# Optimization experiments

Hardware: AMD Instinct MI355X
Metric: run time of the kernel (lower is better)

The kernel has to match this reference:

```python
import jax, jax.numpy as jnp
import numpy as np

N = 80000          # nodes
E = 1280000        # edges (~avg degree 16)
D_IN = 64          # Lorentz ambient dim (1 time + 63 spatial feature dims)
D_HID = 64
EPS = 1e-8


def _lorentz_inner(x):
    # <x,x>_L = -x0^2 + ||x_space||^2  (keepdims)
    return -x[:, :1] * x[:, :1] + jnp.sum(x[:, 1:] * x[:, 1:], axis=-1, keepdims=True)


def _to_manifold(s):
    # scale so that <s,s>_L = -1 (curvature c=1 hyperboloid)
    denom = jnp.sqrt(jnp.clip(jnp.abs(_lorentz_inner(s)), EPS))
    return s / denom


def _lorentz_linear(x, W, b, log_scale, nonlin=None):
    # HyboNet LorentzLinear: dense map, then rebuild a valid hyperboloid point
    if nonlin is not None:
        x = nonlin(x)
    h = x @ W.T + b
    time = jax.nn.sigmoid(h[:, :1]) * jnp.exp(log_scale) + 1.1
    space = h[:, 1:]
    sq = jnp.clip(jnp.sum(space * space, axis=-1, keepdims=True), EPS)
    scale = (time * time - 1.0) / sq
    return jnp.concatenate([time, space * jnp.sqrt(scale)], axis=-1)


def _agg(h, src, dst, w):
    # sparse adjacency aggregation (spmm) + Lorentz centroid normalization
    s = jax.ops.segment_sum(w[:, None] * h[src], dst, num_segments=N)
    return _to_manifold(s)


def setup_inputs() -> dict:
    key = jax.random.key(0)
    ks = jax.random.split(key, 6)
    x = jax.random.normal(ks[0], (N, D_IN - 1), jnp.float32)
    edge_index = jax.random.randint(ks[1], (2, E), 0, N, dtype=jnp.int32)
    edge_weight = jax.random.uniform(ks[2], (E,), jnp.float32)
    W1 = jax.random.normal(ks[3], (D_HID, D_IN), jnp.float32) * 0.02
    b1 = jnp.zeros((D_HID,), jnp.float32)
    s1 = jnp.asarray(np.log(10.0), jnp.float32)   # LorentzLinear scale param (log-space)
    W2 = jax.random.normal(ks[4], (D_HID, D_HID), jnp.float32) * 0.02
    b2 = jnp.zeros((D_HID,), jnp.float32)
    s2 = jnp.asarray(np.log(10.0), jnp.float32)
    return dict(x=x, edge_index=edge_index, edge_weight=edge_weight,
                W1=W1, b1=b1, s1=s1, W2=W2, b2=b2, s2=s2)


def reference(x, edge_index, edge_weight, W1, b1, s1, W2, b2, s2):
    src, dst = edge_index[0], edge_index[1]
    n = x.shape[0]
    # lift to Lorentz tangent space at origin: prepend zero time coord
    # (proj_tan0 is then a no-op since time component is already 0)
    u_space = x                                             # [N, D_IN-1]
    # expmap0 (c=1): [cosh(||u||), sinh(||u||) * u/||u||]
    nrm = jnp.clip(jnp.linalg.norm(u_space, axis=-1, keepdims=True), EPS)
    p_space = jnp.sinh(nrm) * u_space / nrm
    # projx: recompute time coord from spatial part, x0 = sqrt(1 + ||x_s||^2)
    p_time = jnp.sqrt(1.0 + jnp.sum(p_space * p_space, axis=-1, keepdims=True))
    p = jnp.concatenate([p_time, p_space], axis=1)          # [N, D_IN]
    # conv1 (no nonlin) and conv2 (relu) = LorentzLinear + Lorentz aggregation
    h1 = _agg(_lorentz_linear(p, W1, b1, s1), src, dst, edge_weight)
    h2 = _agg(_lorentz_linear(h1, W2, b2, s2, nonlin=jax.nn.relu), src, dst, edge_weight)
    # LResNet hyperbolic residual: Lorentz-normalized sum of the two points
    return _to_manifold(h1 + h2)
```

## Files before the change

### kernel.cpp

```cpp
#include <hip/hip_runtime.h>
#include <hip/hip_bf16.h>

#define D 64
#define EPS 1e-8f
#define BSH 10
#define BNODES (1 << BSH)
#define ABLK 4096

typedef __attribute__((ext_vector_type(8))) short bf16x8;
typedef __attribute__((ext_vector_type(4))) float f32x4;

__device__ __forceinline__ float wave_sum64(float v) {
    #pragma unroll
    for (int d = 1; d < 64; d <<= 1) v += __shfl_xor(v, d);
    return v;
}

__device__ __forceinline__ unsigned short f2bf_rn(float f) {
    unsigned u = __float_as_uint(f);
    return (unsigned short)((u + 0x7FFFu + ((u >> 16) & 1u)) >> 16);
}

__device__ __forceinline__ void split8(float4 a, float4 b, bf16x8& h, bf16x8& l) {
    float f[8] = {a.x, a.y, a.z, a.w, b.x, b.y, b.z, b.w};
    #pragma unroll
    for (int i = 0; i < 8; ++i) {
        unsigned u = __float_as_uint(f[i]);
        float hf = __uint_as_float(u & 0xFFFF0000u);
        unsigned lu = __float_as_uint(f[i] - hf);
        h[i] = (short)(u >> 16);
        l[i] = (short)(lu >> 16);
    }
}

__global__ __launch_bounds__(256) void k_bcount(const int* __restrict__ dst,
                                                int* __restrict__ bcnt,
                                                int e, int nbuck) {
    __shared__ int cnt[128];
    int tid = threadIdx.x;
    if (tid < 128) cnt[tid] = 0;
    __syncthreads();
    int i0 = blockIdx.x * 1024 + tid;
    #pragma unroll
    for (int u = 0; u < 4; ++u) {
        int i = i0 + u * 256;
        if (i < e) atomicAdd(&cnt[dst[i] >> BSH], 1);
    }
    __syncthreads();
    if (tid < nbuck && cnt[tid]) atomicAdd(&bcnt[tid], cnt[tid]);
}

__global__ __launch_bounds__(128) void k_bscan(const int* __restrict__ bcnt,
                                               int* __restrict__ bstart,
                                               int* __restrict__ gcur,
                                               int* __restrict__ off,
                                               int n, int e, int nbuck) {
    __shared__ int sm[128];
    int tid = threadIdx.x;
    int v = (tid < nbuck) ? bcnt[tid] : 0;
    sm[tid] = v;
    __syncthreads();
    #pragma unroll
    for (int d = 1; d < 128; d <<= 1) {
        int t = (tid >= d) ? sm[tid - d] : 0;
        __syncthreads();
        sm[tid] += t;
        __syncthreads();
    }
    int excl = sm[tid] - v;
    if (tid < nbuck) { bstart[tid] = excl; gcur[tid] = excl; }
    if (tid == 0) { bstart[nbuck] = e; off[n] = e; }
}

__global__ __launch_bounds__(256) void k_bucketA(const int* __restrict__ src,
                                                 const int* __restrict__ dst,
                                                 const float* __restrict__ w,
                                                 int* __restrict__ gcur,
                                                 unsigned long long* __restrict__ tmp,
                                                 int e, int nbuck) {
    __shared__ int cnt[128];
    __shared__ int base[128];
    int tid = threadIdx.x;
    if (tid < 128) cnt[tid] = 0;
    __syncthreads();
    int i0 = blockIdx.x * ABLK + tid;
    int bkt[16], rnk[16];
    #pragma unroll
    for (int u = 0; u < 16; ++u) {
        int i = i0 + u * 256;
        if (i < e) {
            int b = dst[i] >> BSH;
            bkt[u] = b;
            rnk[u] = atomicAdd(&cnt[b], 1);
        }
    }
    __syncthreads();
    if (tid < 128) {
        int c = cnt[tid];
        base[tid] = c ? atomicAdd(&gcur[tid], c) : 0;
    }
    __syncthreads();
    #pragma unroll
    for (int u = 0; u < 16; ++u) {
        int i = i0 + u * 256;
        if (i < e) {
            unsigned long long pk =
                ((unsigned long long)__float_as_uint(w[i]) << 32)
                | (unsigned int)(src[i] | ((dst[i] & (BNODES - 1)) << 20));
            tmp[base[bkt[u]] + rnk[u]] = pk;
        }
    }
}

__global__ __launch_bounds__(1024) void k_bucketB(const unsigned long long* __restrict__ tmp,
                                                  const int* __restrict__ bstart,
                                                  int* __restrict__ off,
                                                  unsigned long long* __restrict__ epack,
                                                  int n) {
    __shared__ int cur[BNODES];
    __shared__ int sm[BNODES];
    int b = blockIdx.x;
    int v0 = b << BSH;
    int nv = min(BNODES, n - v0);
    int tid = threadIdx.x;
    cur[tid] = 0;
    __syncthreads();
    int s0 = bstart[b], s1 = bstart[b + 1];
    for (int i = s0 + tid; i < s1; i += 1024)
        atomicAdd(&cur[((unsigned)tmp[i] >> 20) & (BNODES - 1)], 1);
    __syncthreads();
    int v = cur[tid];
    sm[tid] = v;
    __syncthreads();
    #pragma unroll
    for (int d = 1; d < BNODES; d <<= 1) {
        int t = (tid >= d) ? sm[tid - d] : 0;
        __syncthreads();
        sm[tid] += t;
        __syncthreads();
    }
    int node_off = s0 + sm[tid] - v;
    if (tid < nv) off[v0 + tid] = node_off;
    cur[tid] = node_off;
    __syncthreads();
    for (int i = s0 + tid; i < s1; i += 1024) {
        unsigned long long pk = tmp[i];
        int dl = ((unsigned)pk >> 20) & (BNODES - 1);
        int pos = atomicAdd(&cur[dl], 1);
        epack[pos] = pk & 0xFFFFFFFFC00FFFFFULL;
    }
}

__global__ __launch_bounds__(256) void k_embed(const float* __restrict__ x,
                                               float* __restrict__ P, int n) {
    int lane = threadIdx.x & 63, wv = threadIdx.x >> 6;
    int node0 = blockIdx.x * 64 + wv * 16;
    int node1 = min(node0 + 16, n);
    for (int node = node0; node < node1; ++node) {
        float xv = (lane >= 1) ? x[(size_t)node * 63 + (lane - 1)] : 0.f;
        float nrm2 = wave_sum64(xv * xv);
        float nrm = fmaxf(sqrtf(nrm2), EPS);
        float sh = sinhf(nrm);
        float ps = sh * xv / nrm;
        float pt = sqrtf(1.f + sh * sh);
        P[(size_t)node * 64 + lane] = (lane == 0) ? pt : ps;
    }
}

template <int RELU>
__global__ __launch_bounds__(256) void k_lin_mfma(const float* __restrict__ tbl,
                                                  const float* __restrict__ W,
                                                  const float* __restrict__ bias,
                                                  const float* __restrict__ sc,
                                                  unsigned short* __restrict__ out, int n) {
    int lane = threadIdx.x & 63, wv = threadIdx.x >> 6;
    int col = lane & 15, grp = lane >> 4;
    int node0 = blockIdx.x * 64 + wv * 16;
    if (node0 >= n) return;

    float es = expf(sc[0]);

    bf16x8 wh[2][4], wl[2][4];
    #pragma unroll
    for (int s = 0; s < 2; ++s)
        #pragma unroll
        for (int t = 0; t < 4; ++t) {
            const float* wp = W + (t * 16 + col) * 64 + s * 32 + grp * 8;
            split8(*(const float4*)wp, *(const float4*)(wp + 4), wh[s][t], wl[s][t]);
        }

    f32x4 acc[4];
    #pragma unroll
    for (int t = 0; t < 4; ++t) {
        float bv = bias[t * 16 + col];
        acc[t] = (f32x4){bv, bv, bv, bv};
    }

    int arow = node0 + col;
    if (arow >= n) arow = n - 1;
    #pragma unroll
    for (int s = 0; s < 2; ++s) {
        const float* ap = tbl + (size_t)arow * 64 + s * 32 + grp * 8;
        float4 a0 = *(const float4*)ap;
        float4 a1 = *(const float4*)(ap + 4);
        if (RELU) {
            a0.x = fmaxf(a0.x, 0.f); a0.y = fmaxf(a0.y, 0.f);
            a0.z = fmaxf(a0.z, 0.f); a0.w = fmaxf(a0.w, 0.f);
            a1.x = fmaxf(a1.x, 0.f); a1.y = fmaxf(a1.y, 0.f);
            a1.z = fmaxf(a1.z, 0.f); a1.w = fmaxf(a1.w, 0.f);
        }
        bf16x8 ah, al;
        split8(a0, a1, ah, al);
        #pragma unroll
        for (int t = 0; t < 4; ++t) {
            acc[t] = __builtin_amdgcn_mfma_f32_16x16x32_bf16(ah, wh[s][t], acc[t], 0, 0, 0);
            acc[t] = __builtin_amdgcn_mfma_f32_16x16x32_bf16(al, wh[s][t], acc[t], 0, 0, 0);
            acc[t] = __builtin_amdgcn_mfma_f32_16x16x32_bf16(ah, wl[s][t], acc[t], 0, 0, 0);
        }
    }

    float tot[4];
    #pragma unroll
    for (int r = 0; r < 4; ++r) {
        float s = 0.f;
        #pragma unroll
        for (int t = 0; t < 4; ++t) s += acc[t][r] * acc[t][r];
        tot[r] = s;
    }
    #pragma unroll
    for (int d2 = 1; d2 < 16; d2 <<= 1) {
        #pragma unroll
        for (int r = 0; r < 4; ++r) tot[r] += __shfl_xor(tot[r], d2);
    }
    float tm[4], rs[4];
    #pragma unroll
    for (int r = 0; r < 4; ++r) {
        float h0 = __shfl(acc[0][r], lane & 48);
        tm[r] = es / (1.f + expf(-h0)) + 1.1f;
        float sq = fmaxf(tot[r] - h0 * h0, EPS);
        rs[r] = sqrtf((tm[r] * tm[r] - 1.f) / sq);
    }
    #pragma unroll
    for (int t = 0; t < 4; ++t) {
        #pragma unroll
        for (int r = 0; r < 4; ++r) {
            int row = node0 + grp * 4 + r;
            if (row < n) {
                int j = t * 16 + col;
                float v = (j == 0) ? tm[r] : acc[t][r] * rs[r];
                out[(size_t)row * 64 + j] = f2bf_rn(v);
            }
        }
    }
}

template <int FINAL>
__global__ __launch_bounds__(256) void k_agg(const unsigned short* __restrict__ t,
                                             const int* __restrict__ off,
                                             const float2* __restrict__ epack,
                                             const float* __restrict__ h1,
                                             float* __restrict__ out, int n) {
    __shared__ __align__(16) float2 ebuf[4][64];
    int lane = threadIdx.x & 63, wv = threadIdx.x >> 6;
    int q = lane >> 4, sub = lane & 15;
    int node = blockIdx.x * 4 + wv;
    if (node >= n) return;
    int s0 = off[node], s1 = off[node + 1];
    float ax = 0.f, ay = 0.f, az = 0.f, aw = 0.f;
    for (int base = s0; base < s1; base += 64) {
        int c = min(s1 - base, 64);
        float2 ev = (lane < c) ? epack[base + lane] : make_float2(0.f, 0.f);
        ebuf[wv][lane] = ev;
        int c4 = (c + 3) & ~3;
        for (int j = 0; j < c4; j += 4) {
            float2 e = ebuf[wv][j + q];
            int src = __float_as_int(e.x);
            float w = e.y;
            const unsigned* rp = (const unsigned*)(t + ((size_t)src << 6)) + sub * 2;
            uint2 rv = *(const uint2*)rp;
            ax += w * __uint_as_float(rv.x << 16);
            ay += w * __uint_as_float(rv.x & 0xFFFF0000u);
            az += w * __uint_as_float(rv.y << 16);
            aw += w * __uint_as_float(rv.y & 0xFFFF0000u);
        }
    }
    #pragma unroll
    for (int d2 = 16; d2 <= 32; d2 <<= 1) {
        ax += __shfl_xor(ax, d2);
        ay += __shfl_xor(ay, d2);
        az += __shfl_xor(az, d2);
        aw += __shfl_xor(aw, d2);
    }
    float s = ay * ay + az * az + aw * aw;
    s += (sub == 0) ? -ax * ax : ax * ax;
    #pragma unroll
    for (int d2 = 1; d2 < 16; d2 <<= 1) s += __shfl_xor(s, d2);
    float inv = 1.f / sqrtf(fmaxf(fabsf(s), EPS));
    float hx = ax * inv, hy = ay * inv, hz = az * inv, hw = aw * inv;
    if (FINAL) {
        float4 hv = *(const float4*)(h1 + (size_t)node * 64 + sub * 4);
        float vx = hv.x + hx, vy = hv.y + hy, vz = hv.z + hz, vw = hv.w + hw;
        float s2 = vy * vy + vz * vz + vw * vw;
        s2 += (sub == 0) ? -vx * vx : vx * vx;
        #pragma unroll
        for (int d2 = 1; d2 < 16; d2 <<= 1) s2 += __shfl_xor(s2, d2);
        float inv2 = 1.f / sqrtf(fmaxf(fabsf(s2), EPS));
        if (lane < 16) {
            float4 r = make_float4(vx * inv2, vy * inv2, vz * inv2, vw * inv2);
            *(float4*)(out + (size_t)node * 64 + sub * 4) = r;
        }
    } else {
        if (lane < 16) {
            float4 r = make_float4(hx, hy, hz, hw);
            *(float4*)(out + (size_t)node * 64 + sub * 4) = r;
        }
    }
}

extern "C" void kernel_launch(void* const* d_in, const int* in_sizes, int n_in,
                              void* d_out, int out_size, void* d_ws, size_t ws_size,
                              hipStream_t stream) {
    const float* x  = (const float*)d_in[0];
    const int*   ei = (const int*)d_in[1];
    const float* wE = (const float*)d_in[2];
    const float* W1 = (const float*)d_in[3];
    const float* b1 = (const float*)d_in[4];
    const float* s1 = (const float*)d_in[5];
    const float* W2 = (const float*)d_in[6];
    const float* b2 = (const float*)d_in[7];
    const float* s2 = (const float*)d_in[8];
    float* out = (float*)d_out;

    const int N = in_sizes[0] / (D - 1);
    const int E = in_sizes[2];
    const int* src = ei;
    const int* dst = ei + E;
    const int nbuck = (N + BNODES - 1) >> BSH;

    char* ws = (char*)d_ws;
    size_t sz1 = (size_t)N * D * 2;
    size_t szt = (size_t)E * 8;
    if (szt > sz1) sz1 = szt;
    sz1 = (sz1 + 255) & ~(size_t)255;
    unsigned short* T = (unsigned short*)ws;
    unsigned long long* tmp = (unsigned long long*)ws;
    float* B2 = (float*)(ws + sz1);
    unsigned long long* epack = (unsigned long long*)((char*)B2 + (size_t)N * D * 4);
    int* off    = (int*)(epack + E);
    int* bcnt   = off + (N + 1);
    int* bstart = bcnt + 128;
    int* gcur   = bstart + 132;

    hipMemsetAsync(bcnt, 0, 128 * sizeof(int), stream);

    int gE4 = (E + 1023) / 1024;
    int gEA = (E + ABLK - 1) / ABLK;
    int gL = (N + 63) / 64;
    int gA = (N + 3) / 4;

    k_bcount<<<gE4, 256, 0, stream>>>(dst, bcnt, E, nbuck);
    k_bscan<<<1, 128, 0, stream>>>(bcnt, bstart, gcur, off, N, E, nbuck);
    k_bucketA<<<gEA, 256, 0, stream>>>(src, dst, wE, gcur, tmp, E, nbuck);
    k_bucketB<<<nbuck, 1024, 0, stream>>>(tmp, bstart, off, epack, N);

    k_embed<<<gL, 256, 0, stream>>>(x, B2, N);
    k_lin_mfma<0><<<gL, 256, 0, stream>>>(B2, W1, b1, s1, T, N);
    k_agg<0><<<gA, 256, 0, stream>>>(T, off, (const float2*)epack, nullptr, B2, N);
    k_lin_mfma<1><<<gL, 256, 0, stream>>>(B2, W2, b2, s2, T, N);
    k_agg<1><<<gA, 256, 0, stream>>>(T, off, (const float2*)epack, B2, out, N);
}
```

Before: 234.2 us.

## Batch gathers in aggregation, vectorize embed, add nontemporal edge loads/stores

The aggregation kernel now issues up to 16 independent row gathers per 64-edge chunk before accumulating, so more memory loads are in flight per wave. The embed kernel processes four nodes per wave with float4 stores in place of one node per wave iteration. Edge-pack stores and loads, plus the residual h1 read, use nontemporal hints to spare cache capacity for the gathered feature table. The gather buffers raise register pressure, and the source index is now masked to 20 bits out of the packed word.

Measured after the change: 234.4 us. No clear change (+0.1%).

```diff
diff --git a/kernel.cpp b/kernel.cpp
--- a/kernel.cpp
+++ b/kernel.cpp
@@ -147,24 +147,34 @@
         unsigned long long pk = tmp[i];
         int dl = ((unsigned)pk >> 20) & (BNODES - 1);
         int pos = atomicAdd(&cur[dl], 1);
-        epack[pos] = pk & 0xFFFFFFFFC00FFFFFULL;
+        __builtin_nontemporal_store(pk & 0xFFFFFFFFC00FFFFFULL, &epack[pos]);
     }
 }
 
 __global__ __launch_bounds__(256) void k_embed(const float* __restrict__ x,
                                                float* __restrict__ P, int n) {
     int lane = threadIdx.x & 63, wv = threadIdx.x >> 6;
-    int node0 = blockIdx.x * 64 + wv * 16;
-    int node1 = min(node0 + 16, n);
-    for (int node = node0; node < node1; ++node) {
-        float xv = (lane >= 1) ? x[(size_t)node * 63 + (lane - 1)] : 0.f;
-        float nrm2 = wave_sum64(xv * xv);
-        float nrm = fmaxf(sqrtf(nrm2), EPS);
-        float sh = sinhf(nrm);
-        float ps = sh * xv / nrm;
-        float pt = sqrtf(1.f + sh * sh);
-        P[(size_t)node * 64 + lane] = (lane == 0) ? pt : ps;
-    }
+    int q = lane >> 4, sub = lane & 15;
+    int node = blockIdx.x * 16 + wv * 4 + q;
+    if (node >= n) return;
+    const float* xr = x + (size_t)node * 63;
+    float v0 = 0.f, v1, v2, v3;
+    if (sub == 0) {
+        v1 = xr[0]; v2 = xr[1]; v3 = xr[2];
+    } else {
+        int b = sub * 4 - 1;
+        v0 = xr[b]; v1 = xr[b + 1]; v2 = xr[b + 2]; v3 = xr[b + 3];
+    }
+    float s = v0 * v0 + v1 * v1 + v2 * v2 + v3 * v3;
+    #pragma unroll
+    for (int d2 = 1; d2 < 16; d2 <<= 1) s += __shfl_xor(s, d2);
+    float nrm = fmaxf(sqrtf(s), EPS);
+    float sh = sinhf(nrm);
+    float k = sh / nrm;
+    float4 r;
+    if (sub == 0) r = make_float4(sqrtf(1.f + sh * sh), k * v1, k * v2, k * v3);
+    else          r = make_float4(k * v0, k * v1, k * v2, k * v3);
+    *(float4*)(P + (size_t)node * 64 + sub * 4) = r;
 }
 
 template <int RELU>
@@ -257,10 +267,10 @@
 template <int FINAL>
 __global__ __launch_bounds__(256) void k_agg(const unsigned short* __restrict__ t,
                                              const int* __restrict__ off,
-                                             const float2* __restrict__ epack,
+                                             const unsigned long long* __restrict__ epack,
                                              const float* __restrict__ h1,
                                              float* __restrict__ out, int n) {
-    __shared__ __align__(16) float2 ebuf[4][64];
+    __shared__ __align__(16) unsigned long long ebuf[4][64];
     int lane = threadIdx.x & 63, wv = threadIdx.x >> 6;
     int q = lane >> 4, sub = lane & 15;
     int node = blockIdx.x * 4 + wv;
@@ -269,19 +279,29 @@
     float ax = 0.f, ay = 0.f, az = 0.f, aw = 0.f;
     for (int base = s0; base < s1; base += 64) {
         int c = min(s1 - base, 64);
-        float2 ev = (lane < c) ? epack[base + lane] : make_float2(0.f, 0.f);
+        unsigned long long ev = 0;
+        if (lane < c) ev = __builtin_nontemporal_load(&epack[base + lane]);
         ebuf[wv][lane] = ev;
-        int c4 = (c + 3) & ~3;
-        for (int j = 0; j < c4; j += 4) {
-            float2 e = ebuf[wv][j + q];
-            int src = __float_as_int(e.x);
-            float w = e.y;
-            const unsigned* rp = (const unsigned*)(t + ((size_t)src << 6)) + sub * 2;
-            uint2 rv = *(const uint2*)rp;
-            ax += w * __uint_as_float(rv.x << 16);
-            ay += w * __uint_as_float(rv.x & 0xFFFF0000u);
-            az += w * __uint_as_float(rv.y << 16);
-            aw += w * __uint_as_float(rv.y & 0xFFFF0000u);
+        int ng = (c + 3) >> 2;
+        uint2 rv[16]; float wgt[16];
+        #pragma unroll
+        for (int g = 0; g < 16; ++g) {
+            if (g < ng) {
+                unsigned long long e = ebuf[wv][g * 4 + q];
+                wgt[g] = __uint_as_float((unsigned)(e >> 32));
+                unsigned srcn = (unsigned)e & 0xFFFFFu;
+                rv[g] = *(const uint2*)((const unsigned*)(t + ((size_t)srcn << 6)) + sub * 2);
+            }
+        }
+        #pragma unroll
+        for (int g = 0; g < 16; ++g) {
+            if (g < ng) {
+                float w = wgt[g];
+                ax += w * __uint_as_float(rv[g].x << 16);
+                ay += w * __uint_as_float(rv[g].x & 0xFFFF0000u);
+                az += w * __uint_as_float(rv[g].y << 16);
+                aw += w * __uint_as_float(rv[g].y & 0xFFFF0000u);
+            }
         }
     }
     #pragma unroll
@@ -298,8 +318,9 @@
     float inv = 1.f / sqrtf(fmaxf(fabsf(s), EPS));
     float hx = ax * inv, hy = ay * inv, hz = az * inv, hw = aw * inv;
     if (FINAL) {
-        float4 hv = *(const float4*)(h1 + (size_t)node * 64 + sub * 4);
-        float vx = hv.x + hx, vy = hv.y + hy, vz = hv.z + hz, vw = hv.w + hw;
+        f32x4 hv = __builtin_nontemporal_load(
+            (const f32x4*)(h1 + (size_t)node * 64 + sub * 4));
+        float vx = hv[0] + hx, vy = hv[1] + hy, vz = hv[2] + hz, vw = hv[3] + hw;
         float s2 = vy * vy + vz * vz + vw * vw;
         s2 += (sub == 0) ? -vx * vx : vx * vx;
         #pragma unroll
@@ -355,6 +376,7 @@
 
     int gE4 = (E + 1023) / 1024;
     int gEA = (E + ABLK - 1) / ABLK;
+    int gEm = (N + 15) / 16;
     int gL = (N + 63) / 64;
     int gA = (N + 3) / 4;
 
@@ -363,9 +385,9 @@
     k_bucketA<<<gEA, 256, 0, stream>>>(src, dst, wE, gcur, tmp, E, nbuck);
     k_bucketB<<<nbuck, 1024, 0, stream>>>(tmp, bstart, off, epack, N);
 
-    k_embed<<<gL, 256, 0, stream>>>(x, B2, N);
+    k_embed<<<gEm, 256, 0, stream>>>(x, B2, N);
     k_lin_mfma<0><<<gL, 256, 0, stream>>>(B2, W1, b1, s1, T, N);
-    k_agg<0><<<gA, 256, 0, stream>>>(T, off, (const float2*)epack, nullptr, B2, N);
+    k_agg<0><<<gA, 256, 0, stream>>>(T, off, epack, nullptr, B2, N);
     k_lin_mfma<1><<<gL, 256, 0, stream>>>(B2, W2, b2, s2, T, N);
-    k_agg<1><<<gA, 256, 0, stream>>>(T, off, (const float2*)epack, B2, out, N);
-}
+    k_agg<1><<<gA, 256, 0, stream>>>(T, off, epack, B2, out, N);
+}
```
